# Performance work log

Hardware: AMD Instinct MI355X
Metric: run time of the kernel (lower is better)

## Reference

```python
import jax, jax.numpy as jnp
import numpy as np

N_NODES = 80000
N_EDGES = 1280000
NODE_DIM = 32
EDGE_DIM = 16
HIDDEN = 64
N_HIDDEN_LAYERS = 3  # layer_count - 1
NUM_GRAPHS = 256


def setup_inputs() -> dict:
    key = jax.random.key(0)
    ks = jax.random.split(key, 16)
    s = 0.05
    H = jax.random.normal(ks[0], (N_NODES, NODE_DIM), dtype=jnp.float32)
    Xe = jax.random.normal(ks[1], (N_EDGES, EDGE_DIM), dtype=jnp.float32)
    id_Xe = jax.random.randint(ks[2], (2, N_EDGES), 0, N_NODES, dtype=jnp.int32).astype(jnp.int64)
    batch_idx = jnp.sort(jax.random.randint(ks[3], (N_NODES,), 0, NUM_GRAPHS, dtype=jnp.int32)).astype(jnp.int64)
    # input layer: M: (node+edge)->hidden, U: (hidden+node)->hidden
    Mw0 = jax.random.normal(ks[4], (NODE_DIM + EDGE_DIM, HIDDEN), dtype=jnp.float32) * s
    Mb0 = jnp.zeros((HIDDEN,), dtype=jnp.float32)
    Uw0 = jax.random.normal(ks[5], (HIDDEN + NODE_DIM, HIDDEN), dtype=jnp.float32) * s
    Ub0 = jnp.zeros((HIDDEN,), dtype=jnp.float32)
    # hidden layers: M: (hidden+edge)->hidden, U: (2*hidden)->hidden (stacked)
    Mw_h = jax.random.normal(ks[6], (N_HIDDEN_LAYERS, HIDDEN + EDGE_DIM, HIDDEN), dtype=jnp.float32) * s
    Mb_h = jnp.zeros((N_HIDDEN_LAYERS, HIDDEN), dtype=jnp.float32)
    Uw_h = jax.random.normal(ks[7], (N_HIDDEN_LAYERS, 2 * HIDDEN, HIDDEN), dtype=jnp.float32) * s
    Ub_h = jnp.zeros((N_HIDDEN_LAYERS, HIDDEN), dtype=jnp.float32)
    # final linear head hidden -> 1
    Ww = jax.random.normal(ks[8], (HIDDEN, 1), dtype=jnp.float32) * s
    Wb = jnp.zeros((1,), dtype=jnp.float32)
    return {"H": H, "Xe": Xe, "id_Xe": id_Xe, "batch_idx": batch_idx,
            "Mw0": Mw0, "Mb0": Mb0, "Uw0": Uw0, "Ub0": Ub0,
            "Mw_h": Mw_h, "Mb_h": Mb_h, "Uw_h": Uw_h, "Ub_h": Ub_h,
            "Ww": Ww, "Wb": Wb}


def reference(H, Xe, id_Xe, batch_idx, Mw0, Mb0, Uw0, Ub0, Mw_h, Mb_h, Uw_h, Ub_h, Ww, Wb):
    n = H.shape[0]
    src = id_Xe[0]
    dst = id_Xe[1]

    def gnn_layer(h, Mw, Mb, Uw, Ub):
        # message: gather source node features, concat edge features, MLP M
        m = jax.nn.relu(jnp.concatenate([h[src], Xe], axis=-1) @ Mw + Mb)  # [E, hidden]
        # scatter-sum to target nodes
        agg = jax.ops.segment_sum(m, dst, num_segments=n)  # [N, hidden]
        # update: concat node state with aggregated message, MLP U
        return jax.nn.relu(jnp.concatenate([h, agg], axis=-1) @ Uw + Ub)

    y = gnn_layer(H, Mw0, Mb0, Uw0, Ub0)
    for i in range(Mw_h.shape[0]):
        y = gnn_layer(y, Mw_h[i], Mb_h[i], Uw_h[i], Ub_h[i])

    pooled = jax.ops.segment_sum(y, batch_idx, num_segments=NUM_GRAPHS)  # [G, hidden]
    return pooled @ Ww + Wb  # [G, 1]
```

## Files before the change

### kernel.cpp

```cpp
#include <hip/hip_runtime.h>
#include <hip/hip_fp16.h>

#define HID 64

struct alignas(8)  H4 { __half2 a, b; };
struct alignas(16) H8 { __half2 h[4]; };

typedef _Float16 h2n __attribute__((ext_vector_type(2)));

__device__ inline float dot2f(__half2 a, __half2 b, float c) {
#if __has_builtin(__builtin_amdgcn_fdot2)
    h2n an, bn;
    __builtin_memcpy(&an, &a, 4);
    __builtin_memcpy(&bn, &b, 4);
    return __builtin_amdgcn_fdot2(an, bn, c, false);
#else
    float2 af = __half22float2(a), bf = __half22float2(b);
    return c + af.x * bf.x + af.y * bf.y;
#endif
}

__global__ __launch_bounds__(256) void deg_count(const int* __restrict__ dst,
                                                 int* __restrict__ deg, int E) {
    int e = blockIdx.x * 256 + threadIdx.x;
    if (e < E) atomicAdd(&deg[dst[e]], 1);
}

__global__ __launch_bounds__(256) void scan1(const int* __restrict__ deg,
                                             int* __restrict__ rowptr,
                                             int* __restrict__ bsums, int N) {
    __shared__ int s[256];
    const int t = threadIdx.x;
    const int base = blockIdx.x * 2048 + t * 8;
    int v[8], tot = 0;
    #pragma unroll
    for (int i = 0; i < 8; i++) {
        int x = (base + i < N) ? deg[base + i] : 0;
        v[i] = tot; tot += x;
    }
    s[t] = tot; __syncthreads();
    for (int off = 1; off < 256; off <<= 1) {
        int a = (t >= off) ? s[t - off] : 0;
        __syncthreads(); s[t] += a; __syncthreads();
    }
    const int texcl = s[t] - tot;
    #pragma unroll
    for (int i = 0; i < 8; i++)
        if (base + i < N) rowptr[base + i] = texcl + v[i];
    if (t == 255) bsums[blockIdx.x] = s[255];
}

__global__ void scan2(int* bsums, int NB) {
    if (blockIdx.x == 0 && threadIdx.x == 0) {
        int run = 0;
        for (int i = 0; i < NB; i++) { int x = bsums[i]; bsums[i] = run; run += x; }
    }
}

__global__ __launch_bounds__(256) void scan3(int* __restrict__ rowptr,
                                             const int* __restrict__ bsums,
                                             int N, int E) {
    int idx = blockIdx.x * 256 + threadIdx.x;
    if (idx < N) rowptr[idx] += bsums[idx >> 11];
    if (idx == 0) rowptr[N] = E;
}

__global__ __launch_bounds__(256) void permute_k(
    const int* __restrict__ src, const int* __restrict__ dst,
    const int* __restrict__ rowptr, int* __restrict__ cursor,
    const float* __restrict__ Xe, __half* __restrict__ Xes,
    unsigned* __restrict__ pks, int E)
{
    int e = blockIdx.x * 256 + threadIdx.x;
    if (e >= E) return;
    int d = dst[e];
    int pos = rowptr[d] + atomicAdd(&cursor[d], 1);
    pks[pos] = ((unsigned)src[e] << 5) | (unsigned)(d & 31);
    const float4* xi = (const float4*)&Xe[(size_t)e * 16];
    float4 x0 = xi[0], x1 = xi[1], x2 = xi[2], x3 = xi[3];
    H8 h0, h1;
    h0.h[0] = __float22half2_rn(make_float2(x0.x, x0.y));
    h0.h[1] = __float22half2_rn(make_float2(x0.z, x0.w));
    h0.h[2] = __float22half2_rn(make_float2(x1.x, x1.y));
    h0.h[3] = __float22half2_rn(make_float2(x1.z, x1.w));
    h1.h[0] = __float22half2_rn(make_float2(x2.x, x2.y));
    h1.h[1] = __float22half2_rn(make_float2(x2.z, x2.w));
    h1.h[2] = __float22half2_rn(make_float2(x3.x, x3.y));
    h1.h[3] = __float22half2_rn(make_float2(x3.z, x3.w));
    H8* xo = (H8*)&Xes[(size_t)pos * 16];
    xo[0] = h0; xo[1] = h1;
}

template<int K1>
__global__ __launch_bounds__(256) void pm_dual(
    const float* __restrict__ Hn,
    const float* __restrict__ Wm, const float* __restrict__ bm,
    const float* __restrict__ Wu, const float* __restrict__ bu,
    __half* __restrict__ PMh, __half* __restrict__ Th, int N)
{
    constexpr int KP = K1 + 4;
    constexpr int P4 = K1 / 4;
    __shared__ float Ws[K1 * 128];
    __shared__ float Xs[32 * KP];

    const int tid = threadIdx.x;
    for (int i = tid; i < K1 * 32; i += 256) {
        const int row = i >> 5, c4 = i & 31;
        float4 v = (c4 < 16) ? *(const float4*)&Wm[row * 64 + c4 * 4]
                             : *(const float4*)&Wu[row * 64 + (c4 - 16) * 4];
        *(float4*)&Ws[row * 128 + c4 * 4] = v;
    }
    const int nbase = blockIdx.x * 32;
    for (int i = tid; i < 32 * P4; i += 256) {
        const int nl = i / P4, part = i % P4;
        const int n = nbase + nl;
        if (n < N)
            *(float4*)&Xs[nl * KP + part * 4] =
                *(const float4*)&Hn[(size_t)n * K1 + part * 4];
    }
    __syncthreads();

    const int c0 = (tid & 31) * 4;
    const int n0 = (tid >> 5) * 4;
    const float4 bv = (c0 < 64) ? *(const float4*)&bm[c0]
                                : *(const float4*)&bu[c0 - 64];

    float4 acc[4];
    #pragma unroll
    for (int i = 0; i < 4; i++) acc[i] = bv;

    #pragma unroll 4
    for (int k = 0; k < K1; k += 4) {
        const float4 w0 = *(const float4*)&Ws[(k + 0) * 128 + c0];
        const float4 w1 = *(const float4*)&Ws[(k + 1) * 128 + c0];
        const float4 w2 = *(const float4*)&Ws[(k + 2) * 128 + c0];
        const float4 w3 = *(const float4*)&Ws[(k + 3) * 128 + c0];
        #pragma unroll
        for (int ni = 0; ni < 4; ni++) {
            const float4 xv = *(const float4*)&Xs[(n0 + ni) * KP + k];
            acc[ni].x += xv.x * w0.x + xv.y * w1.x + xv.z * w2.x + xv.w * w3.x;
            acc[ni].y += xv.x * w0.y + xv.y * w1.y + xv.z * w2.y + xv.w * w3.y;
            acc[ni].z += xv.x * w0.z + xv.y * w1.z + xv.z * w2.z + xv.w * w3.z;
            acc[ni].w += xv.x * w0.w + xv.y * w1.w + xv.z * w2.w + xv.w * w3.w;
        }
    }

    #pragma unroll
    for (int ni = 0; ni < 4; ni++) {
        const int n = nbase + n0 + ni;
        if (n < N) {
            H4 o;
            o.a = __float22half2_rn(make_float2(acc[ni].x, acc[ni].y));
            o.b = __float22half2_rn(make_float2(acc[ni].z, acc[ni].w));
            if (c0 < 64) *(H4*)&PMh[(size_t)n * 64 + c0]      = o;
            else         *(H4*)&Th [(size_t)n * 64 + c0 - 64] = o;
        }
    }
}

__global__ __launch_bounds__(256) void edge_fused(
    const __half*   __restrict__ PMh,
    const __half*   __restrict__ Th,
    const __half*   __restrict__ Xes,
    const unsigned* __restrict__ pks,
    const int*      __restrict__ rowptr,
    const float*    __restrict__ Mwb,
    const float*    __restrict__ Uwb,
    float*          __restrict__ Yout,
    int N)
{
    constexpr int AGP = HID + 4;
    __shared__ float aggs[32 * AGP];

    const int tid  = threadIdx.x;
    const int wv   = tid >> 6;
    const int lane = tid & 63;
    const int c0   = (lane & 15) * 4;
    const int g    = lane >> 4;

    __half2 wh[8][4];
    #pragma unroll
    for (int p = 0; p < 8; p++)
        #pragma unroll
        for (int j = 0; j < 4; j++)
            wh[p][j] = __float22half2_rn(make_float2(Mwb[(2 * p) * 64 + c0 + j],
                                                     Mwb[(2 * p + 1) * 64 + c0 + j]));

    for (int i = tid; i < 32 * AGP; i += 256) aggs[i] = 0.f;

    const int nbase  = blockIdx.x * 32;
    const int nend   = (nbase + 32 < N) ? nbase + 32 : N;
    const int estart = rowptr[nbase];
    const int eend   = rowptr[nend];
    __syncthreads();

    int pc = estart + wv * 16;
    unsigned pk_c[4], pk_n[4], pk_n2[4];
    H4 ph_c[4], ph_n[4];
    H8 xh_c[4][2], xh_n[4][2];

    if (pc < eend) {
        #pragma unroll
        for (int s = 0; s < 4; s++) {
            const int pe = pc + g * 4 + s;
            pk_c[s] = pks[pe < eend ? pe : eend - 1];
        }
        if (pc + 64 < eend) {
            #pragma unroll
            for (int s = 0; s < 4; s++) {
                const int pe = pc + 64 + g * 4 + s;
                pk_n[s] = pks[pe < eend ? pe : eend - 1];
            }
        }
        #pragma unroll
        for (int s = 0; s < 4; s++) {
            const int pe  = pc + g * 4 + s;
            const int pcl = pe < eend ? pe : eend - 1;
            ph_c[s] = *(const H4*)&PMh[(size_t)(pk_c[s] >> 5) * 64 + c0];
            const H8* xr = (const H8*)&Xes[(size_t)pcl * 16];
            xh_c[s][0] = xr[0]; xh_c[s][1] = xr[1];
        }
    }

    for (; pc < eend; pc += 64) {
        const int pn  = pc + 64;
        const int pn2 = pc + 128;

        if (pn < eend) {
            #pragma unroll
            for (int s = 0; s < 4; s++) {
                const int pe  = pn + g * 4 + s;
                const int pcl = pe < eend ? pe : eend - 1;
                ph_n[s] = *(const H4*)&PMh[(size_t)(pk_n[s] >> 5) * 64 + c0];
                const H8* xr = (const H8*)&Xes[(size_t)pcl * 16];
                xh_n[s][0] = xr[0]; xh_n[s][1] = xr[1];
            }
        }
        if (pn2 < eend) {
            #pragma unroll
            for (int s = 0; s < 4; s++) {
                const int pe = pn2 + g * 4 + s;
                pk_n2[s] = pks[pe < eend ? pe : eend - 1];
            }
        }

        int ld_prev = -1;
        float4 racc = make_float4(0.f, 0.f, 0.f, 0.f);
        #pragma unroll
        for (int s = 0; s < 4; s++) {
            const bool valid = (pc + g * 4 + s) < eend;
            const float2 pl = __half22float2(ph_c[s].a);
            const float2 pu = __half22float2(ph_c[s].b);
            float a0 = pl.x, a1 = pl.y, a2 = pu.x, a3 = pu.y;
            #pragma unroll
            for (int p = 0; p < 8; p++) {
                const __half2 xv = xh_c[s][p >> 2].h[p & 3];
                a0 = dot2f(xv, wh[p][0], a0);
                a1 = dot2f(xv, wh[p][1], a1);
                a2 = dot2f(xv, wh[p][2], a2);
                a3 = dot2f(xv, wh[p][3], a3);
            }
            float4 v;
            v.x = fmaxf(a0, 0.f); v.y = fmaxf(a1, 0.f);
            v.z = fmaxf(a2, 0.f); v.w = fmaxf(a3, 0.f);
            const int ld = valid ? (int)(pk_c[s] & 31u) : -1;
            if (ld == ld_prev) {
                racc.x += v.x; racc.y += v.y; racc.z += v.z; racc.w += v.w;
            } else {
                if (ld_prev >= 0) {
                    float* a = &aggs[ld_prev * AGP + c0];
                    atomicAdd(a + 0, racc.x); atomicAdd(a + 1, racc.y);
                    atomicAdd(a + 2, racc.z); atomicAdd(a + 3, racc.w);
                }
                racc = v; ld_prev = ld;
            }
        }
        if (ld_prev >= 0) {
            float* a = &aggs[ld_prev * AGP + c0];
            atomicAdd(a + 0, racc.x); atomicAdd(a + 1, racc.y);
            atomicAdd(a + 2, racc.z); atomicAdd(a + 3, racc.w);
        }

        #pragma unroll
        for (int s = 0; s < 4; s++) {
            pk_c[s] = pk_n[s]; pk_n[s] = pk_n2[s];
            ph_c[s] = ph_n[s];
            xh_c[s][0] = xh_n[s][0]; xh_c[s][1] = xh_n[s][1];
        }
    }

    __syncthreads();

    {
        const int c0t = (tid & 15) * 4;
        const int r0  = tid >> 4;
        const int r1  = r0 + 16;
        const int n0g = nbase + r0, n1g = nbase + r1;
        float4 acc0 = make_float4(0.f, 0.f, 0.f, 0.f);
        float4 acc1 = make_float4(0.f, 0.f, 0.f, 0.f);
        if (n0g < N) {
            H4 th = *(const H4*)&Th[(size_t)n0g * 64 + c0t];
            float2 lo = __half22float2(th.a), hi = __half22float2(th.b);
            acc0 = make_float4(lo.x, lo.y, hi.x, hi.y);
        }
        if (n1g < N) {
            H4 th = *(const H4*)&Th[(size_t)n1g * 64 + c0t];
            float2 lo = __half22float2(th.a), hi = __half22float2(th.b);
            acc1 = make_float4(lo.x, lo.y, hi.x, hi.y);
        }
        #pragma unroll 4
        for (int k = 0; k < 64; k += 4) {
            const float4 w0 = *(const float4*)&Uwb[(k + 0) * 64 + c0t];
            const float4 w1 = *(const float4*)&Uwb[(k + 1) * 64 + c0t];
            const float4 w2 = *(const float4*)&Uwb[(k + 2) * 64 + c0t];
            const float4 w3 = *(const float4*)&Uwb[(k + 3) * 64 + c0t];
            const float4 x0 = *(const float4*)&aggs[r0 * AGP + k];
            const float4 x1 = *(const float4*)&aggs[r1 * AGP + k];
            acc0.x += x0.x * w0.x + x0.y * w1.x + x0.z * w2.x + x0.w * w3.x;
            acc0.y += x0.x * w0.y + x0.y * w1.y + x0.z * w2.y + x0.w * w3.y;
            acc0.z += x0.x * w0.z + x0.y * w1.z + x0.z * w2.z + x0.w * w3.z;
            acc0.w += x0.x * w0.w + x0.y * w1.w + x0.z * w2.w + x0.w * w3.w;
            acc1.x += x1.x * w0.x + x1.y * w1.x + x1.z * w2.x + x1.w * w3.x;
            acc1.y += x1.x * w0.y + x1.y * w1.y + x1.z * w2.y + x1.w * w3.y;
            acc1.z += x1.x * w0.z + x1.y * w1.z + x1.z * w2.z + x1.w * w3.z;
            acc1.w += x1.x * w0.w + x1.y * w1.w + x1.z * w2.w + x1.w * w3.w;
        }
        if (n0g < N) {
            float4 o;
            o.x = fmaxf(acc0.x, 0.f); o.y = fmaxf(acc0.y, 0.f);
            o.z = fmaxf(acc0.z, 0.f); o.w = fmaxf(acc0.w, 0.f);
            *(float4*)&Yout[(size_t)n0g * HID + c0t] = o;
        }
        if (n1g < N) {
            float4 o;
            o.x = fmaxf(acc1.x, 0.f); o.y = fmaxf(acc1.y, 0.f);
            o.z = fmaxf(acc1.z, 0.f); o.w = fmaxf(acc1.w, 0.f);
            *(float4*)&Yout[(size_t)n1g * HID + c0t] = o;
        }
    }
}

__global__ __launch_bounds__(256) void pool_head(
    const float* __restrict__ Y, const int* __restrict__ bidx,
    const float* __restrict__ Ww, const float* __restrict__ Wb,
    float* __restrict__ out, int N)
{
    const int g = blockIdx.x;
    int a = 0, b = N;
    while (a < b) { int m = (a + b) >> 1; if (bidx[m] < g) a = m + 1; else b = m; }
    const int lo = a;
    b = N;
    while (a < b) { int m = (a + b) >> 1; if (bidx[m] < g + 1) a = m + 1; else b = m; }
    const int hi = a;

    const int tid = threadIdx.x;
    const int c4 = tid & 15, nl = tid >> 4;
    float4 s = make_float4(0.f, 0.f, 0.f, 0.f);
    for (int n = lo + nl; n < hi; n += 16) {
        const float4 v = *(const float4*)&Y[(size_t)n * HID + c4 * 4];
        s.x += v.x; s.y += v.y; s.z += v.z; s.w += v.w;
    }
    __shared__ float red[16 * 68];
    *(float4*)&red[nl * 68 + c4 * 4] = s;
    __syncthreads();
    if (tid < 64) {
        float t = 0.f;
        #pragma unroll
        for (int r = 0; r < 16; r++) t += red[r * 68 + tid];
        t *= Ww[tid];
        #pragma unroll
        for (int off = 32; off; off >>= 1) t += __shfl_down(t, off);
        if (tid == 0) out[g] = t + Wb[0];
    }
}

extern "C" void kernel_launch(void* const* d_in, const int* in_sizes, int n_in,
                              void* d_out, int out_size, void* d_ws, size_t ws_size,
                              hipStream_t stream) {
    const float* H    = (const float*)d_in[0];
    const float* Xe   = (const float*)d_in[1];
    const int*   ids  = (const int*)d_in[2];
    const int*   bidx = (const int*)d_in[3];
    const float* Mw0  = (const float*)d_in[4];
    const float* Mb0  = (const float*)d_in[5];
    const float* Uw0  = (const float*)d_in[6];
    const float* Ub0  = (const float*)d_in[7];
    const float* MwH  = (const float*)d_in[8];
    const float* MbH  = (const float*)d_in[9];
    const float* UwH  = (const float*)d_in[10];
    const float* UbH  = (const float*)d_in[11];
    const float* Ww   = (const float*)d_in[12];
    const float* Wb   = (const float*)d_in[13];
    float* out = (float*)d_out;

    const int N = in_sizes[0] / 32;
    const int E = in_sizes[1] / 16;
    const int* src = ids;
    const int* dst = ids + E;

    float*  hbuf = (float*)d_ws;
    __half* PMh  = (__half*)(hbuf + (size_t)N * HID);
    __half* Th   = PMh + (size_t)N * HID;
    __half* Xes  = Th  + (size_t)N * HID;
    unsigned* pks = (unsigned*)(Xes + (size_t)E * 16);
    int* rowptr  = (int*)(pks + E);
    int* deg     = rowptr + (N + 1);
    int* bsums   = deg + N;

    const int NB = (N + 2047) / 2048;
    const int eblocks = (E + 255) / 256;
    const int ntile   = (N + 31) / 32;

    hipMemsetAsync(deg, 0, (size_t)N * sizeof(int), stream);
    deg_count<<<eblocks, 256, 0, stream>>>(dst, deg, E);
    scan1<<<NB, 256, 0, stream>>>(deg, rowptr, bsums, N);
    scan2<<<1, 64, 0, stream>>>(bsums, NB);
    scan3<<<(N + 255) / 256, 256, 0, stream>>>(rowptr, bsums, N, E);
    hipMemsetAsync(deg, 0, (size_t)N * sizeof(int), stream);
    permute_k<<<eblocks, 256, 0, stream>>>(src, dst, rowptr, deg,
                                           Xe, Xes, pks, E);

    pm_dual<32><<<ntile, 256, 0, stream>>>(H, Mw0, Mb0, Uw0, Ub0, PMh, Th, N);
    edge_fused<<<ntile, 256, 0, stream>>>(PMh, Th, Xes, pks, rowptr,
                                          Mw0 + 32 * HID, Uw0 + 32 * HID, hbuf, N);

    for (int l = 0; l < 3; l++) {
        const float* Mw = MwH + (size_t)l * 80 * HID;
        const float* Uw = UwH + (size_t)l * 128 * HID;
        pm_dual<64><<<ntile, 256, 0, stream>>>(hbuf, Mw, MbH + (size_t)l * HID,
                                               Uw, UbH + (size_t)l * HID, PMh, Th, N);
        edge_fused<<<ntile, 256, 0, stream>>>(PMh, Th, Xes, pks, rowptr,
                                              Mw + 64 * HID, Uw + 64 * HID, hbuf, N);
    }

    pool_head<<<256, 256, 0, stream>>>(hbuf, bidx, Ww, Wb, out, N);
}
```

Before: 964.8 us.

## Compute edge message MLP with MFMA, folding gathered node projection via identity

Replaces the per-lane fdot2 message computation in the fused edge kernel with four mfma_f32_16x16x32_f16 ops per 16-edge tile. The K dimension is made from the 16 edge features plus the gathered 16-column slice of the precomputed node projection, and the B fragment holds an identity block so that slice is added in. Edge-group indices are read once per lane and broadcast with shuffles. The scatter to shared-memory aggregation is reorganised to the MFMA output layout. The aim is to cut VALU work per edge. The cost is a different gather pattern, and edge-feature rows past the segment end are read without clamping.

```diff
diff --git a/kernel.cpp b/kernel.cpp
--- a/kernel.cpp
+++ b/kernel.cpp
@@ -6,19 +6,8 @@
 struct alignas(8)  H4 { __half2 a, b; };
 struct alignas(16) H8 { __half2 h[4]; };
 
-typedef _Float16 h2n __attribute__((ext_vector_type(2)));
-
-__device__ inline float dot2f(__half2 a, __half2 b, float c) {
-#if __has_builtin(__builtin_amdgcn_fdot2)
-    h2n an, bn;
-    __builtin_memcpy(&an, &a, 4);
-    __builtin_memcpy(&bn, &b, 4);
-    return __builtin_amdgcn_fdot2(an, bn, c, false);
-#else
-    float2 af = __half22float2(a), bf = __half22float2(b);
-    return c + af.x * bf.x + af.y * bf.y;
-#endif
-}
+typedef _Float16 f16x8 __attribute__((ext_vector_type(8)));
+typedef float    f32x4 __attribute__((ext_vector_type(4)));
 
 __global__ __launch_bounds__(256) void deg_count(const int* __restrict__ dst,
                                                  int* __restrict__ deg, int E) {
@@ -175,16 +164,22 @@
     const int tid  = threadIdx.x;
     const int wv   = tid >> 6;
     const int lane = tid & 63;
-    const int c0   = (lane & 15) * 4;
-    const int g    = lane >> 4;
-
-    __half2 wh[8][4];
+    const int n    = lane & 15;
+    const int quad = lane >> 4;
+
+    f16x8 bfrag[4];
     #pragma unroll
-    for (int p = 0; p < 8; p++)
-        #pragma unroll
-        for (int j = 0; j < 4; j++)
-            wh[p][j] = __float22half2_rn(make_float2(Mwb[(2 * p) * 64 + c0 + j],
-                                                     Mwb[(2 * p + 1) * 64 + c0 + j]));
+    for (int s = 0; s < 4; s++) {
+        f16x8 b;
+        #pragma unroll
+        for (int jj = 0; jj < 8; jj++) {
+            const int k = quad * 8 + jj;
+            float w = (k < 16) ? Mwb[k * 64 + 16 * s + n]
+                               : ((k - 16) == n ? 1.f : 0.f);
+            b[jj] = (_Float16)w;
+        }
+        bfrag[s] = b;
+    }
 
     for (int i = tid; i < 32 * AGP; i += 256) aggs[i] = 0.f;
 
@@ -195,98 +190,82 @@
     __syncthreads();
 
     int pc = estart + wv * 16;
-    unsigned pk_c[4], pk_n[4], pk_n2[4];
-    H4 ph_c[4], ph_n[4];
-    H8 xh_c[4][2], xh_n[4][2];
+    unsigned spk_c = 0, spk_n = 0, spk_n2 = 0;
+    f16x8 af_c[4], af_n[4];
+
+    auto loadA = [&](int p0, unsigned spk, f16x8* af) {
+        const __half* xbase = Xes + (size_t)(p0 + n) * 16 + quad * 8;
+        const __half* pbase = PMh + (size_t)(spk >> 5) * 64 + (quad - 2) * 8;
+        #pragma unroll
+        for (int s = 0; s < 4; s++) {
+            const __half* p = (quad < 2) ? xbase : (pbase + 16 * s);
+            af[s] = *(const f16x8*)p;
+        }
+    };
 
     if (pc < eend) {
-        #pragma unroll
-        for (int s = 0; s < 4; s++) {
-            const int pe = pc + g * 4 + s;
-            pk_c[s] = pks[pe < eend ? pe : eend - 1];
+        {
+            const int pe = pc + n;
+            spk_c = pks[pe < eend ? pe : eend - 1];
         }
         if (pc + 64 < eend) {
-            #pragma unroll
-            for (int s = 0; s < 4; s++) {
-                const int pe = pc + 64 + g * 4 + s;
-                pk_n[s] = pks[pe < eend ? pe : eend - 1];
-            }
-        }
-        #pragma unroll
-        for (int s = 0; s < 4; s++) {
-            const int pe  = pc + g * 4 + s;
-            const int pcl = pe < eend ? pe : eend - 1;
-            ph_c[s] = *(const H4*)&PMh[(size_t)(pk_c[s] >> 5) * 64 + c0];
-            const H8* xr = (const H8*)&Xes[(size_t)pcl * 16];
-            xh_c[s][0] = xr[0]; xh_c[s][1] = xr[1];
-        }
+            const int pe = pc + 64 + n;
+            spk_n = pks[pe < eend ? pe : eend - 1];
+        }
+        loadA(pc, spk_c, af_c);
     }
 
     for (; pc < eend; pc += 64) {
         const int pn  = pc + 64;
         const int pn2 = pc + 128;
 
-        if (pn < eend) {
-            #pragma unroll
-            for (int s = 0; s < 4; s++) {
-                const int pe  = pn + g * 4 + s;
-                const int pcl = pe < eend ? pe : eend - 1;
-                ph_n[s] = *(const H4*)&PMh[(size_t)(pk_n[s] >> 5) * 64 + c0];
-                const H8* xr = (const H8*)&Xes[(size_t)pcl * 16];
-                xh_n[s][0] = xr[0]; xh_n[s][1] = xr[1];
+        if (pn < eend) loadA(pn, spk_n, af_n);
+        if (pn2 < eend) {
+            const int pe = pn2 + n;
+            spk_n2 = pks[pe < eend ? pe : eend - 1];
+        }
+
+        int qld[4];
+        #pragma unroll
+        for (int r = 0; r < 4; r++)
+            qld[r] = (int)(__shfl(spk_c, quad * 4 + r) & 31u);
+
+        f32x4 acc[4];
+        #pragma unroll
+        for (int s = 0; s < 4; s++)
+            acc[s] = __builtin_amdgcn_mfma_f32_16x16x32_f16(
+                af_c[s], bfrag[s], (f32x4){0.f, 0.f, 0.f, 0.f}, 0, 0, 0);
+
+        int ldp = -1;
+        float rs0 = 0.f, rs1 = 0.f, rs2 = 0.f, rs3 = 0.f;
+        #pragma unroll
+        for (int r = 0; r < 4; r++) {
+            const bool valid = (pc + quad * 4 + r) < eend;
+            const int ld = valid ? qld[r] : -1;
+            const float v0 = fmaxf(acc[0][r], 0.f);
+            const float v1 = fmaxf(acc[1][r], 0.f);
+            const float v2 = fmaxf(acc[2][r], 0.f);
+            const float v3 = fmaxf(acc[3][r], 0.f);
+            if (ld == ldp) {
+                rs0 += v0; rs1 += v1; rs2 += v2; rs3 += v3;
+            } else {
+                if (ldp >= 0) {
+                    float* a = &aggs[ldp * AGP + n];
+                    atomicAdd(a +  0, rs0); atomicAdd(a + 16, rs1);
+                    atomicAdd(a + 32, rs2); atomicAdd(a + 48, rs3);
+                }
+                rs0 = v0; rs1 = v1; rs2 = v2; rs3 = v3; ldp = ld;
             }
         }
-        if (pn2 < eend) {
-            #pragma unroll
-            for (int s = 0; s < 4; s++) {
-                const int pe = pn2 + g * 4 + s;
-                pk_n2[s] = pks[pe < eend ? pe : eend - 1];
-            }
-        }
-
-        int ld_prev = -1;
-        float4 racc = make_float4(0.f, 0.f, 0.f, 0.f);
-        #pragma unroll
-        for (int s = 0; s < 4; s++) {
-            const bool valid = (pc + g * 4 + s) < eend;
-            const float2 pl = __half22float2(ph_c[s].a);
-            const float2 pu = __half22float2(ph_c[s].b);
-            float a0 = pl.x, a1 = pl.y, a2 = pu.x, a3 = pu.y;
-            #pragma unroll
-            for (int p = 0; p < 8; p++) {
-                const __half2 xv = xh_c[s][p >> 2].h[p & 3];
-                a0 = dot2f(xv, wh[p][0], a0);
-                a1 = dot2f(xv, wh[p][1], a1);
-                a2 = dot2f(xv, wh[p][2], a2);
-                a3 = dot2f(xv, wh[p][3], a3);
-            }
-            float4 v;
-            v.x = fmaxf(a0, 0.f); v.y = fmaxf(a1, 0.f);
-            v.z = fmaxf(a2, 0.f); v.w = fmaxf(a3, 0.f);
-            const int ld = valid ? (int)(pk_c[s] & 31u) : -1;
-            if (ld == ld_prev) {
-                racc.x += v.x; racc.y += v.y; racc.z += v.z; racc.w += v.w;
-            } else {
-                if (ld_prev >= 0) {
-                    float* a = &aggs[ld_prev * AGP + c0];
-                    atomicAdd(a + 0, racc.x); atomicAdd(a + 1, racc.y);
-                    atomicAdd(a + 2, racc.z); atomicAdd(a + 3, racc.w);
-                }
-                racc = v; ld_prev = ld;
-            }
-        }
-        if (ld_prev >= 0) {
-            float* a = &aggs[ld_prev * AGP + c0];
-            atomicAdd(a + 0, racc.x); atomicAdd(a + 1, racc.y);
-            atomicAdd(a + 2, racc.z); atomicAdd(a + 3, racc.w);
-        }
-
-        #pragma unroll
-        for (int s = 0; s < 4; s++) {
-            pk_c[s] = pk_n[s]; pk_n[s] = pk_n2[s];
-            ph_c[s] = ph_n[s];
-            xh_c[s][0] = xh_n[s][0]; xh_c[s][1] = xh_n[s][1];
-        }
+        if (ldp >= 0) {
+            float* a = &aggs[ldp * AGP + n];
+            atomicAdd(a +  0, rs0); atomicAdd(a + 16, rs1);
+            atomicAdd(a + 32, rs2); atomicAdd(a + 48, rs3);
+        }
+
+        spk_c = spk_n; spk_n = spk_n2;
+        #pragma unroll
+        for (int s = 0; s < 4; s++) af_c[s] = af_n[s];
     }
 
     __syncthreads();
```

New measurement: 972.5 us. Within noise of the previous version (+0.8%).
